# Kernel optimization log

Hardware: AMD Instinct MI355X
Metric: run time of the kernel (lower is better)

The kernel has to match this reference:

```python
import jax, jax.numpy as jnp
import numpy as np

B, LATENT, P, NUM_ATOMS, H, L, E = 16, 128, 16, 64, 64, 4, 32768
N = P * NUM_ATOMS  # 1024

def _lin(k, i, o, s=0.05):
    kw, kb = jax.random.split(k)
    return jax.random.normal(kw, (i, o), jnp.float32) * s, jax.random.normal(kb, (o,), jnp.float32) * s

def setup_inputs() -> dict:
    key = jax.random.key(0)
    ks = jax.random.split(key, 32)
    z = jax.random.normal(ks[0], (B, LATENT), jnp.float32)
    edge_index = jax.random.randint(ks[1], (2, E), 0, N, jnp.int32)
    # build_node_features: (frame/P, atom/num_atoms, 1) per node
    fr = jnp.repeat(jnp.arange(P), NUM_ATOMS) / P
    at = jnp.tile(jnp.arange(NUM_ATOMS), P) / NUM_ATOMS
    node_features = jnp.stack([fr, at, jnp.ones(N)], -1).astype(jnp.float32)
    Wg, bg = _lin(ks[2], LATENT, H)
    Wn, bn = _lin(ks[3], 3, H)
    def stack(fn, base):
        outs = [fn(jax.random.fold_in(key, base + l)) for l in range(L)]
        return tuple(jnp.stack(t) for t in zip(*outs))
    eW1, eb1 = stack(lambda k: _lin(k, 2 * H + 1, H), 100)
    eW2, eb2 = stack(lambda k: _lin(k, H, H), 200)
    cW1, cb1 = stack(lambda k: _lin(k, H, H), 300)
    cW2 = jnp.stack([jax.random.normal(jax.random.fold_in(key, 400 + l), (H, 1), jnp.float32) * 0.05 for l in range(L)])
    nW1, nb1 = stack(lambda k: _lin(k, 2 * H, H), 500)
    nW2, nb2 = stack(lambda k: _lin(k, H, H), 600)
    lng = jnp.ones((L, H), jnp.float32)
    lnb = jnp.zeros((L, H), jnp.float32)
    oW1, ob1 = _lin(ks[4], H, H)
    oW2, ob2 = _lin(ks[5], H, 3)
    return dict(z=z, edge_index=edge_index, node_features=node_features, Wg=Wg, bg=bg, Wn=Wn, bn=bn,
                eW1=eW1, eb1=eb1, eW2=eW2, eb2=eb2, cW1=cW1, cb1=cb1, cW2=cW2,
                nW1=nW1, nb1=nb1, nW2=nW2, nb2=nb2, lng=lng, lnb=lnb,
                oW1=oW1, ob1=ob1, oW2=oW2, ob2=ob2)

def _forward(z, edge_index, node_features, Wg, bg, Wn, bn, eW1, eb1, eW2, eb2,
             cW1, cb1, cW2, nW1, nb1, nW2, nb2, lng, lnb, oW1, ob1, oW2, ob2):
    b = z.shape[0]
    n = node_features.shape[0]
    row, col = edge_index[0], edge_index[1]  # aggregate messages to row
    counts = jnp.clip(jnp.zeros((n,), jnp.float32).at[row].add(1.0), 1.0, None)
    g = z @ Wg + bg                              # [B,H]
    h = (node_features @ Wn + bn)[None] + g[:, None]  # [B,N,H]
    pos = jnp.zeros((b, n, 3), h.dtype)
    for l in range(L):
        hi, hj = h[:, row], h[:, col]            # [B,E,H] gathers
        diff = pos[:, row] - pos[:, col]         # [B,E,3]
        d2 = jnp.sum(diff * diff, -1, keepdims=True)
        m = jax.nn.silu(jnp.concatenate([hi, hj, d2], -1) @ eW1[l] + eb1[l])
        m = jax.nn.silu(m @ eW2[l] + eb2[l])     # [B,E,H]
        w = jax.nn.silu(m @ cW1[l] + cb1[l]) @ cW2[l]  # [B,E,1]
        trans = diff * w
        pos = pos + jnp.zeros_like(pos).at[:, row].add(trans) / counts[None, :, None]
        agg = jnp.zeros_like(h).at[:, row].add(m)      # scatter-sum to nodes
        u = jax.nn.silu(jnp.concatenate([h, agg], -1) @ nW1[l] + nb1[l]) @ nW2[l] + nb2[l]
        h = h + u                                 # node residual
        mu = jnp.mean(h, -1, keepdims=True)
        var = jnp.mean((h - mu) ** 2, -1, keepdims=True)
        h = (h - mu) * jax.lax.rsqrt(var + 1e-5) * lng[l] + lnb[l]
    out = jax.nn.relu(h @ oW1 + ob1) @ oW2 + ob2   # [B,N,3]
    return out.reshape(b, -1)

def reference(z, edge_index, node_features, Wg, bg, Wn, bn, eW1, eb1, eW2, eb2,
              cW1, cb1, cW2, nW1, nb1, nW2, nb2, lng, lnb, oW1, ob1, oW2, ob2):
    return _forward(z, edge_index, node_features, Wg, bg, Wn, bn, eW1, eb1, eW2, eb2,
                    cW1, cb1, cW2, nW1, nb1, nW2, nb2, lng, lnb, oW1, ob1, oW2, ob2)
```

## Files before the change

kernel.cpp:

```cpp
#include <hip/hip_runtime.h>
#include <hip/hip_bf16.h>


namespace {

constexpr int kB = 16, kN = 1024, kH = 64, kE = 32768, kLat = 128;
constexpr int kC = 24;
constexpr int kMaxItems = 2560;

typedef __attribute__((ext_vector_type(8))) short short8;
typedef __attribute__((ext_vector_type(4))) float floatx4;

__device__ __forceinline__ unsigned short f2bf(float f){
  union { float f; unsigned int u; } v; v.f = f;
  unsigned int r = v.u + 0x7fffu + ((v.u >> 16) & 1u);
  return (unsigned short)(r >> 16);
}
__device__ __forceinline__ unsigned int packbf(float a, float b){
  return ((unsigned int)f2bf(b) << 16) | (unsigned int)f2bf(a);
}
__device__ __forceinline__ unsigned int pack2f(float a, float b){
  unsigned int ua = __float_as_uint(a) + 0x8000u;
  unsigned int ub = __float_as_uint(b) + 0x8000u;
  return __builtin_amdgcn_perm(ub, ua, 0x07060302);
}
__device__ __forceinline__ float bflo(unsigned int u){
  union { unsigned int u; float f; } v; v.u = u << 16; return v.f;
}
__device__ __forceinline__ float bfhi(unsigned int u){
  union { unsigned int u; float f; } v; v.u = u & 0xffff0000u; return v.f;
}
__device__ __forceinline__ float silu2(float x){
  float u = __builtin_amdgcn_exp2f(-1.44269504f * x);
  return x * __builtin_amdgcn_rcpf(1.0f + u);
}

__global__ void k_count(const int* ei, int* cntI){
  int e = blockIdx.x*256 + threadIdx.x;
  atomicAdd(&cntI[ei[e]], 1);
}

__global__ void k_scan(const int* cntI, int* off, int* ioff, int* fill,
                       int* items, int* nitems){
  __shared__ int s0[1024];
  __shared__ int s1[1024];
  int t = threadIdx.x;
  int c = cntI[t];
  s0[t] = c; __syncthreads();
  int* src = s0; int* dst = s1;
  for (int o = 1; o < 1024; o <<= 1){
    int v = src[t] + ((t >= o) ? src[t-o] : 0);
    dst[t] = v; __syncthreads();
    int* tmp = src; src = dst; dst = tmp;
  }
  int inc = src[t];
  off[t] = inc - c;
  if (t == 1023) off[1024] = inc;
  fill[t] = 0;
  int ic = (c + (kC-1)) / kC;
  __syncthreads();
  s0[t] = ic; __syncthreads();
  src = s0; dst = s1;
  for (int o = 1; o < 1024; o <<= 1){
    int v = src[t] + ((t >= o) ? src[t-o] : 0);
    dst[t] = v; __syncthreads();
    int* tmp = src; src = dst; dst = tmp;
  }
  int inc2 = src[t];
  int ib = inc2 - ic;
  ioff[t] = ib;
  if (t == 1023){ ioff[1024] = inc2; *nitems = inc2; }
  for (int s = 0; s < ic; s++) items[ib + s] = (t << 12) | s;
}

__global__ void k_bucket(const int* ei, const int* off, int* fill, int* ecol,
                         const float* eW2, unsigned short* wfragE,
                         const float* z, const float* Wg, const float* bg,
                         float* g){
  int e = blockIdx.x*256 + threadIdx.x;
  int r = ei[e];
  int s = atomicAdd(&fill[r], 1);
  ecol[off[r] + s] = ei[kE + e];
  if (blockIdx.x < 4){
    int l = blockIdx.x;
    for (int i = threadIdx.x; i < 4096; i += 256){
      int f = i >> 9, lane = (i >> 3) & 63, j8 = i & 7;
      int jt = f >> 1, ks = f & 1;
      int k = ks*32 + (lane >> 4)*8 + j8;
      int j = jt*16 + (lane & 15);
      wfragE[l*4096 + i] = f2bf(eW2[l*4096 + k*64 + j]);
    }
  } else if (blockIdx.x < 8){
    int b = (blockIdx.x - 4)*4 + (threadIdx.x >> 6);
    int j = threadIdx.x & 63;
    float acc = bg[j];
    for (int k = 0; k < kLat; k++) acc += z[b*kLat + k] * Wg[k*64 + j];
    g[b*64 + j] = acc;
  }
}

__global__ __launch_bounds__(256, 3) void k_pre(const float* nf, const float* Wn,
      const float* bn, const float* g, const float* eW1, const float* eb1,
      float* h, float* A1t, unsigned short* A2bf){
  __shared__ __align__(16) float W0[4096];
  __shared__ __align__(16) float W1[4096];
  __shared__ __align__(16) float HR[16*68];
  __shared__ float b1s[64];
  int tid = threadIdx.x;
  int bb = blockIdx.x >> 6;
  int n0 = (blockIdx.x & 63) * 16;
  {
    const float4* e1a = (const float4*)(eW1);
    const float4* e1b = (const float4*)(eW1 + 4096);
    for (int i = tid; i < 1024; i += 256){ ((float4*)W0)[i] = e1a[i]; ((float4*)W1)[i] = e1b[i]; }
  }
  if (tid < 64) b1s[tid] = eb1[tid];
  int rl = tid >> 4, c = tid & 15, j0 = c*4;
  int n = n0 + rl;
  int row = bb*1024 + n;
  float f0 = nf[n*3], f1 = nf[n*3+1], f2 = nf[n*3+2];
  float4 hv;
  hv.x = f0*Wn[j0+0] + f1*Wn[64+j0+0] + f2*Wn[128+j0+0] + bn[j0+0] + g[bb*64+j0+0];
  hv.y = f0*Wn[j0+1] + f1*Wn[64+j0+1] + f2*Wn[128+j0+1] + bn[j0+1] + g[bb*64+j0+1];
  hv.z = f0*Wn[j0+2] + f1*Wn[64+j0+2] + f2*Wn[128+j0+2] + bn[j0+2] + g[bb*64+j0+2];
  hv.w = f0*Wn[j0+3] + f1*Wn[64+j0+3] + f2*Wn[128+j0+3] + bn[j0+3] + g[bb*64+j0+3];
  *(float4*)(h + row*64 + j0) = hv;
  *(float4*)(HR + rl*68 + j0) = hv;
  __syncthreads();
  float4 a1 = { b1s[j0], b1s[j0+1], b1s[j0+2], b1s[j0+3] };
  float4 a2 = { 0.f, 0.f, 0.f, 0.f };
  #pragma unroll 8
  for (int k = 0; k < 64; k++){
    float hk = HR[rl*68 + k];
    float4 w1 = *(const float4*)(W0 + k*64 + j0);
    float4 w2 = *(const float4*)(W1 + k*64 + j0);
    a1.x += hk*w1.x; a1.y += hk*w1.y; a1.z += hk*w1.z; a1.w += hk*w1.w;
    a2.x += hk*w2.x; a2.y += hk*w2.y; a2.z += hk*w2.z; a2.w += hk*w2.w;
  }
  int tb = (n*16 + bb)*64;
  *(float4*)(A1t + tb + j0) = a1;
  uint2 pk; pk.x = packbf(a2.x, a2.y); pk.y = packbf(a2.z, a2.w);
  *(uint2*)(A2bf + tb + j0) = pk;
}

__global__ __launch_bounds__(256, 3) void k_edge(const float* A1t,
      const unsigned short* A2bf, const unsigned short* wfragE,
      const float* eb2, int l, const int* off, const int* ecol,
      const int* items, const int* nitems, float* P){
  int w = blockIdx.x*4 + (threadIdx.x >> 6);
  if (w >= *nitems) return;
  int lane = threadIdx.x & 63;
  int m = lane & 15, quad = lane >> 4;
  int it = items[w];
  int r = it >> 12, s = it & 4095;
  int e0 = off[r] + s*kC;
  int e1 = min(off[r+1], e0 + kC);

  short8 wf[8];
  #pragma unroll
  for (int f = 0; f < 8; f++)
    wf[f] = *(const short8*)(wfragE + l*4096 + f*512 + lane*8);

  float4 a1[4];
  #pragma unroll
  for (int ks = 0; ks < 2; ks++){
    a1[ks*2+0] = *(const float4*)(A1t + (r<<10) + (m<<6) + ks*32 + quad*8);
    a1[ks*2+1] = *(const float4*)(A1t + (r<<10) + (m<<6) + ks*32 + quad*8 + 4);
  }
  floatx4 dini[4];
  #pragma unroll
  for (int jt = 0; jt < 4; jt++)
    dini[jt] = *(const floatx4*)(eb2 + l*64 + jt*16 + quad*4);
  floatx4 agg[4];
  #pragma unroll
  for (int jt = 0; jt < 4; jt++) agg[jt] = (floatx4){0.f,0.f,0.f,0.f};

  int c0 = ecol[e0];
  uint4 p0 = *(const uint4*)(A2bf + ((c0<<4)+m)*64 + quad*8);
  uint4 p1 = *(const uint4*)(A2bf + ((c0<<4)+m)*64 + 32 + quad*8);

  for (int e = e0; e < e1; e++){
    uint4 c_0 = p0, c_1 = p1;
    if (e + 1 < e1){
      int cn = ecol[e+1];
      p0 = *(const uint4*)(A2bf + ((cn<<4)+m)*64 + quad*8);
      p1 = *(const uint4*)(A2bf + ((cn<<4)+m)*64 + 32 + quad*8);
    }
    short8 bfr[2];
    #pragma unroll
    for (int ks = 0; ks < 2; ks++){
      uint4 a2r = (ks == 0) ? c_0 : c_1;
      float4 x0 = a1[ks*2+0];
      float4 x1 = a1[ks*2+1];
      float v0 = silu2(x0.x + bflo(a2r.x));
      float v1 = silu2(x0.y + bfhi(a2r.x));
      float v2 = silu2(x0.z + bflo(a2r.y));
      float v3 = silu2(x0.w + bfhi(a2r.y));
      float v4 = silu2(x1.x + bflo(a2r.z));
      float v5 = silu2(x1.y + bfhi(a2r.z));
      float v6 = silu2(x1.z + bflo(a2r.w));
      float v7 = silu2(x1.w + bfhi(a2r.w));
      union { uint4 u; short8 s; } bu;
      bu.u.x = pack2f(v0, v1); bu.u.y = pack2f(v2, v3);
      bu.u.z = pack2f(v4, v5); bu.u.w = pack2f(v6, v7);
      bfr[ks] = bu.s;
    }
    #pragma unroll
    for (int jt = 0; jt < 4; jt++){
      floatx4 d = dini[jt];
      d = __builtin_amdgcn_mfma_f32_16x16x32_bf16(wf[jt*2+0], bfr[0], d, 0, 0, 0);
      d = __builtin_amdgcn_mfma_f32_16x16x32_bf16(wf[jt*2+1], bfr[1], d, 0, 0, 0);
      floatx4 a = agg[jt];
      a.x += silu2(d.x); a.y += silu2(d.y);
      a.z += silu2(d.z); a.w += silu2(d.w);
      agg[jt] = a;
    }
  }
  #pragma unroll
  for (int jt = 0; jt < 4; jt++)
    *(floatx4*)(P + w*1024 + m*64 + jt*16 + quad*4) = agg[jt];
}

template <bool LAST>
__global__ __launch_bounds__(256, 3) void k_post(int l, float* h, const float* P,
      const int* ioff, const float* nW1, const float* nb1_, const float* nW2,
      const float* nb2_, const float* lng_, const float* lnb_,
      const float* eW1, const float* eb1_, float* A1t, unsigned short* A2bf,
      const float* oW1, const float* ob1_, const float* oW2, const float* ob2_,
      float* out){
  __shared__ __align__(16) float W0[4096];
  __shared__ __align__(16) float W1[4096];
  __shared__ __align__(16) float HR[16*68];
  __shared__ __align__(16) float AG[16*68];
  __shared__ __align__(16) float TL[16*68];
  __shared__ float b1s[64], b2s[64], lgs[64], lbs[64];
  __shared__ float W2o[192];
  __shared__ float ob2s[4];
  int tid = threadIdx.x;
  int bb = blockIdx.x >> 6;
  int n0 = (blockIdx.x & 63) * 16;
  int rl = tid >> 4, c = tid & 15, j0 = c*4;
  int n = n0 + rl;
  int row = bb*1024 + n;

  {
    const float4* p1 = (const float4*)(nW1 + l*8192);
    const float4* p2 = (const float4*)(nW1 + l*8192 + 4096);
    for (int i = tid; i < 1024; i += 256){ ((float4*)W0)[i] = p1[i]; ((float4*)W1)[i] = p2[i]; }
  }
  if (tid < 64){
    b1s[tid] = nb1_[l*64+tid]; b2s[tid] = nb2_[l*64+tid];
    lgs[tid] = lng_[l*64+tid]; lbs[tid] = lnb_[l*64+tid];
  }
  {
    float4 hv = *(const float4*)(h + row*64 + j0);
    *(float4*)(HR + rl*68 + j0) = hv;
    float4 s = {0.f,0.f,0.f,0.f};
    int i0 = ioff[n], i1 = ioff[n+1];
    for (int i = i0; i < i1; i++){
      float4 v = *(const float4*)(P + i*1024 + bb*64 + j0);
      s.x += v.x; s.y += v.y; s.z += v.z; s.w += v.w;
    }
    *(float4*)(AG + rl*68 + j0) = s;
  }
  __syncthreads();

  float4 t = { b1s[j0], b1s[j0+1], b1s[j0+2], b1s[j0+3] };
  #pragma unroll 8
  for (int k = 0; k < 64; k++){
    float hk = HR[rl*68 + k], ak = AG[rl*68 + k];
    float4 w1 = *(const float4*)(W0 + k*64 + j0);
    float4 w2 = *(const float4*)(W1 + k*64 + j0);
    t.x += hk*w1.x + ak*w2.x; t.y += hk*w1.y + ak*w2.y;
    t.z += hk*w1.z + ak*w2.z; t.w += hk*w1.w + ak*w2.w;
  }
  t.x = silu2(t.x); t.y = silu2(t.y); t.z = silu2(t.z); t.w = silu2(t.w);
  *(float4*)(TL + rl*68 + j0) = t;
  __syncthreads();

  {
    const float4* p3 = (const float4*)(nW2 + l*4096);
    for (int i = tid; i < 1024; i += 256) ((float4*)W0)[i] = p3[i];
  }
  __syncthreads();

  float4 u = { b2s[j0], b2s[j0+1], b2s[j0+2], b2s[j0+3] };
  #pragma unroll 8
  for (int k = 0; k < 64; k++){
    float tk = TL[rl*68 + k];
    float4 w = *(const float4*)(W0 + k*64 + j0);
    u.x += tk*w.x; u.y += tk*w.y; u.z += tk*w.z; u.w += tk*w.w;
  }
  float4 hold = *(const float4*)(HR + rl*68 + j0);
  float4 hv = { hold.x + u.x, hold.y + u.y, hold.z + u.z, hold.w + u.w };
  float s1 = hv.x + hv.y + hv.z + hv.w;
  float s2 = hv.x*hv.x + hv.y*hv.y + hv.z*hv.z + hv.w*hv.w;
  s1 += __shfl_xor(s1, 1, 64); s1 += __shfl_xor(s1, 2, 64);
  s1 += __shfl_xor(s1, 4, 64); s1 += __shfl_xor(s1, 8, 64);
  s2 += __shfl_xor(s2, 1, 64); s2 += __shfl_xor(s2, 2, 64);
  s2 += __shfl_xor(s2, 4, 64); s2 += __shfl_xor(s2, 8, 64);
  float mu  = s1 * (1.0f/64.0f);
  float var = s2 * (1.0f/64.0f) - mu*mu;
  float rs  = rsqrtf(var + 1e-5f);
  float4 hn;
  hn.x = (hv.x-mu)*rs*lgs[j0+0] + lbs[j0+0];
  hn.y = (hv.y-mu)*rs*lgs[j0+1] + lbs[j0+1];
  hn.z = (hv.z-mu)*rs*lgs[j0+2] + lbs[j0+2];
  hn.w = (hv.w-mu)*rs*lgs[j0+3] + lbs[j0+3];
  if (!LAST) *(float4*)(h + row*64 + j0) = hn;
  *(float4*)(HR + rl*68 + j0) = hn;
  __syncthreads();

  if (!LAST){
    {
      const float4* e1a = (const float4*)(eW1 + (l+1)*8256);
      const float4* e1b = (const float4*)(eW1 + (l+1)*8256 + 4096);
      for (int i = tid; i < 1024; i += 256){ ((float4*)W0)[i] = e1a[i]; ((float4*)W1)[i] = e1b[i]; }
    }
    if (tid < 64) b1s[tid] = eb1_[(l+1)*64 + tid];
    __syncthreads();
    float4 a1 = { b1s[j0], b1s[j0+1], b1s[j0+2], b1s[j0+3] };
    float4 a2 = { 0.f, 0.f, 0.f, 0.f };
    #pragma unroll 8
    for (int k = 0; k < 64; k++){
      float hk = HR[rl*68 + k];
      float4 w1 = *(const float4*)(W0 + k*64 + j0);
      float4 w2 = *(const float4*)(W1 + k*64 + j0);
      a1.x += hk*w1.x; a1.y += hk*w1.y; a1.z += hk*w1.z; a1.w += hk*w1.w;
      a2.x += hk*w2.x; a2.y += hk*w2.y; a2.z += hk*w2.z; a2.w += hk*w2.w;
    }
    int tb = (n*16 + bb)*64;
    *(float4*)(A1t + tb + j0) = a1;
    uint2 pk; pk.x = packbf(a2.x, a2.y); pk.y = packbf(a2.z, a2.w);
    *(uint2*)(A2bf + tb + j0) = pk;
  } else {
    {
      const float4* w1p = (const float4*)oW1;
      for (int i = tid; i < 1024; i += 256) ((float4*)W0)[i] = w1p[i];
    }
    if (tid < 192) W2o[tid] = oW2[tid];
    if (tid < 64)  b1s[tid] = ob1_[tid];
    if (tid < 3)   ob2s[tid] = ob2_[tid];
    __syncthreads();
    float4 tr = { b1s[j0], b1s[j0+1], b1s[j0+2], b1s[j0+3] };
    #pragma unroll 8
    for (int k = 0; k < 64; k++){
      float hk = HR[rl*68 + k];
      float4 w = *(const float4*)(W0 + k*64 + j0);
      tr.x += hk*w.x; tr.y += hk*w.y; tr.z += hk*w.z; tr.w += hk*w.w;
    }
    float4 t4 = { fmaxf(tr.x,0.f), fmaxf(tr.y,0.f), fmaxf(tr.z,0.f), fmaxf(tr.w,0.f) };
    *(float4*)(TL + rl*68 + j0) = t4;
    __syncthreads();
    if (c < 3){
      float acc = ob2s[c];
      #pragma unroll 8
      for (int k = 0; k < 64; k++) acc += TL[rl*68 + k] * W2o[k*3 + c];
      out[bb*3072 + n*3 + c] = acc;
    }
  }
}

}

extern "C" void kernel_launch(void* const* d_in, const int* in_sizes, int n_in,
                              void* d_out, int out_size, void* d_ws, size_t ws_size,
                              hipStream_t stream){
  const float* z   = (const float*)d_in[0];
  const int*   ei  = (const int*)d_in[1];
  const float* nf  = (const float*)d_in[2];
  const float* Wg  = (const float*)d_in[3];  const float* bg  = (const float*)d_in[4];
  const float* Wn  = (const float*)d_in[5];  const float* bn  = (const float*)d_in[6];
  const float* eW1 = (const float*)d_in[7];  const float* eb1 = (const float*)d_in[8];
  const float* eW2 = (const float*)d_in[9];  const float* eb2 = (const float*)d_in[10];
  const float* nW1 = (const float*)d_in[14]; const float* nb1 = (const float*)d_in[15];
  const float* nW2 = (const float*)d_in[16]; const float* nb2 = (const float*)d_in[17];
  const float* lng = (const float*)d_in[18]; const float* lnb = (const float*)d_in[19];
  const float* oW1 = (const float*)d_in[20]; const float* ob1 = (const float*)d_in[21];
  const float* oW2 = (const float*)d_in[22]; const float* ob2 = (const float*)d_in[23];

  float* W      = (float*)d_ws;
  float* h      = W;
  float* A1t    = W + 1048576;
  unsigned short* A2bf   = (unsigned short*)(W + 2097152);
  unsigned short* wfragE = (unsigned short*)(W + 2621440);
  float* P      = W + 2629632;
  float* g      = W + 5251072;
  int*   cntI   = (int*)(W + 5252096);
  int*   off    = cntI + 1024;
  int*   ioff   = off + 1025;
  int*   fill   = ioff + 1025;
  int*   items  = fill + 1024;
  int*   nitems = items + 2560;
  int*   ecol   = nitems + 1;

  hipMemsetAsync(cntI, 0, 1024*sizeof(int), stream);
  k_count <<<128, 256, 0, stream>>>(ei, cntI);
  k_scan  <<<1,  1024, 0, stream>>>(cntI, off, ioff, fill, items, nitems);
  k_bucket<<<128, 256, 0, stream>>>(ei, off, fill, ecol, eW2, wfragE, z, Wg, bg, g);
  k_pre   <<<1024, 256, 0, stream>>>(nf, Wn, bn, g, eW1, eb1, h, A1t, A2bf);

  for (int l = 0; l < 4; l++){
    k_edge<<<640, 256, 0, stream>>>(A1t, A2bf, wfragE, eb2, l, off, ecol,
                                    items, nitems, P);
    if (l < 3)
      k_post<false><<<1024, 256, 0, stream>>>(l, h, P, ioff, nW1, nb1, nW2, nb2,
            lng, lnb, eW1, eb1, A1t, A2bf, oW1, ob1, oW2, ob2, (float*)d_out);
    else
      k_post<true> <<<1024, 256, 0, stream>>>(l, h, P, ioff, nW1, nb1, nW2, nb2,
            lng, lnb, eW1, eb1, A1t, A2bf, oW1, ob1, oW2, ob2, (float*)d_out);
  }
}
```

Baseline: 366.9 us.

## Fuse whole forward into one persistent cooperative kernel with grid syncs

Replaces the sequence of count/scan/bucket/pre/edge/post launches with a single cooperative kernel of 768 blocks. Phases are separated by grid-wide syncs and use grid-stride loops over work items. The aim is to remove per-launch overhead and inter-kernel gaps across roughly eleven launches. In exchange, the edge and node phases run on fewer blocks, the scan runs on a single block while the rest wait, and the grid barriers add their own cost. The old multi-kernel path is kept as a fallback if the cooperative launch fails.

```diff
diff --git a/kernel.cpp b/kernel.cpp
--- a/kernel.cpp
+++ b/kernel.cpp
@@ -1,12 +1,15 @@
 #include <hip/hip_runtime.h>
 #include <hip/hip_bf16.h>
+#include <hip/hip_cooperative_groups.h>
+
+namespace cg = cooperative_groups;
 
 
 namespace {
 
 constexpr int kB = 16, kN = 1024, kH = 64, kE = 32768, kLat = 128;
 constexpr int kC = 24;
-constexpr int kMaxItems = 2560;
+constexpr int kGrid = 768;
 
 typedef __attribute__((ext_vector_type(8))) short short8;
 typedef __attribute__((ext_vector_type(4))) float floatx4;
@@ -33,6 +36,326 @@
 __device__ __forceinline__ float silu2(float x){
   float u = __builtin_amdgcn_exp2f(-1.44269504f * x);
   return x * __builtin_amdgcn_rcpf(1.0f + u);
+}
+
+struct Params {
+  const float *z, *nf, *Wg, *bg, *Wn, *bn, *eW1, *eb1, *eW2, *eb2;
+  const float *nW1, *nb1, *nW2, *nb2, *lng, *lnb, *oW1, *ob1, *oW2, *ob2;
+  const int *ei;
+  float *h, *A1t, *P, *g, *out;
+  unsigned short *A2bf, *wfragE;
+  int *cntI, *off, *ioff, *fill, *items, *nitems, *ecol;
+};
+
+__global__ __launch_bounds__(256, 3) void k_all(Params p){
+  __shared__ __align__(16) float W0[4096];
+  __shared__ __align__(16) float W1[4096];
+  __shared__ __align__(16) float HR[16*68];
+  __shared__ __align__(16) float AG[16*68];
+  __shared__ float b1s[64], b2s[64], lgs[64], lbs[64];
+  __shared__ float W2o[192];
+  __shared__ float ob2s[4];
+
+  cg::grid_group gg = cg::this_grid();
+  const int tid = threadIdx.x, blk = blockIdx.x;
+  const int rl = tid >> 4, cc = tid & 15, j0 = cc*4;
+  const int wav = tid >> 6, lane = tid & 63;
+  const int m = lane & 15, quad = lane >> 4;
+
+  for (int e = blk*256 + tid; e < kE; e += kGrid*256)
+    atomicAdd(&p.cntI[p.ei[e]], 1);
+  if (blk < 4){
+    int l = blk;
+    for (int i = tid; i < 4096; i += 256){
+      int f = i >> 9, ln = (i >> 3) & 63, j8 = i & 7;
+      int jt = f >> 1, ks = f & 1;
+      int k = ks*32 + (ln >> 4)*8 + j8;
+      int j = jt*16 + (ln & 15);
+      p.wfragE[l*4096 + i] = f2bf(p.eW2[l*4096 + k*64 + j]);
+    }
+  } else if (blk == 4){
+    int j = tid & 63, b0 = tid >> 6;
+    for (int b = b0; b < 16; b += 4){
+      float acc = p.bg[j];
+      for (int k = 0; k < kLat; k++) acc += p.z[b*kLat + k] * p.Wg[k*64 + j];
+      p.g[b*64 + j] = acc;
+    }
+  }
+  gg.sync();
+
+  if (blk == 0){
+    int* s0 = (int*)W0; int* s1 = s0 + 1024;
+    for (int i = tid; i < 1024; i += 256) s0[i] = p.cntI[i];
+    __syncthreads();
+    int* src = s0; int* dst = s1;
+    for (int o = 1; o < 1024; o <<= 1){
+      for (int i = tid; i < 1024; i += 256)
+        dst[i] = src[i] + ((i >= o) ? src[i-o] : 0);
+      __syncthreads();
+      int* t = src; src = dst; dst = t;
+    }
+    for (int i = tid; i < 1024; i += 256){
+      int c = p.cntI[i];
+      p.off[i] = c ? (src[i] - c) : src[i];
+      p.off[i] = src[i] - c;
+      p.fill[i] = 0;
+    }
+    if (tid == 0) p.off[1024] = src[1023];
+    __syncthreads();
+    for (int i = tid; i < 1024; i += 256) dst[i] = (p.cntI[i] + kC - 1)/kC;
+    __syncthreads();
+    int* src2 = dst; int* dst2 = src;
+    for (int o = 1; o < 1024; o <<= 1){
+      for (int i = tid; i < 1024; i += 256)
+        dst2[i] = src2[i] + ((i >= o) ? src2[i-o] : 0);
+      __syncthreads();
+      int* t = src2; src2 = dst2; dst2 = t;
+    }
+    for (int i = tid; i < 1024; i += 256){
+      int ic = (p.cntI[i] + kC - 1)/kC;
+      int ib = src2[i] - ic;
+      p.ioff[i] = ib;
+      for (int s = 0; s < ic; s++) p.items[ib + s] = (i << 12) | s;
+    }
+    if (tid == 0){ p.ioff[1024] = src2[1023]; p.nitems[0] = src2[1023]; }
+  }
+  gg.sync();
+
+  for (int e = blk*256 + tid; e < kE; e += kGrid*256){
+    int r = p.ei[e];
+    int s = atomicAdd(&p.fill[r], 1);
+    p.ecol[p.off[r] + s] = p.ei[kE + e];
+  }
+  gg.sync();
+
+  {
+    const float4* e1a = (const float4*)(p.eW1);
+    const float4* e1b = (const float4*)(p.eW1 + 4096);
+    for (int i = tid; i < 1024; i += 256){ ((float4*)W0)[i] = e1a[i]; ((float4*)W1)[i] = e1b[i]; }
+    if (tid < 64) b1s[tid] = p.eb1[tid];
+    __syncthreads();
+    for (int grp = blk; grp < 1024; grp += kGrid){
+      int bb = grp >> 6, n0 = (grp & 63)*16;
+      int n = n0 + rl, row = bb*1024 + n;
+      float f0 = p.nf[n*3], f1 = p.nf[n*3+1], f2 = p.nf[n*3+2];
+      float4 hv;
+      hv.x = f0*p.Wn[j0+0] + f1*p.Wn[64+j0+0] + f2*p.Wn[128+j0+0] + p.bn[j0+0] + p.g[bb*64+j0+0];
+      hv.y = f0*p.Wn[j0+1] + f1*p.Wn[64+j0+1] + f2*p.Wn[128+j0+1] + p.bn[j0+1] + p.g[bb*64+j0+1];
+      hv.z = f0*p.Wn[j0+2] + f1*p.Wn[64+j0+2] + f2*p.Wn[128+j0+2] + p.bn[j0+2] + p.g[bb*64+j0+2];
+      hv.w = f0*p.Wn[j0+3] + f1*p.Wn[64+j0+3] + f2*p.Wn[128+j0+3] + p.bn[j0+3] + p.g[bb*64+j0+3];
+      *(float4*)(p.h + row*64 + j0) = hv;
+      *(float4*)(HR + rl*68 + j0) = hv;
+      __syncthreads();
+      float4 a1 = { b1s[j0], b1s[j0+1], b1s[j0+2], b1s[j0+3] };
+      float4 a2 = { 0.f, 0.f, 0.f, 0.f };
+      #pragma unroll 8
+      for (int k = 0; k < 64; k++){
+        float hk = HR[rl*68 + k];
+        float4 w1 = *(const float4*)(W0 + k*64 + j0);
+        float4 w2 = *(const float4*)(W1 + k*64 + j0);
+        a1.x += hk*w1.x; a1.y += hk*w1.y; a1.z += hk*w1.z; a1.w += hk*w1.w;
+        a2.x += hk*w2.x; a2.y += hk*w2.y; a2.z += hk*w2.z; a2.w += hk*w2.w;
+      }
+      int tb = (n*16 + bb)*64;
+      *(float4*)(p.A1t + tb + j0) = a1;
+      uint2 pk2; pk2.x = packbf(a2.x, a2.y); pk2.y = packbf(a2.z, a2.w);
+      *(uint2*)(p.A2bf + tb + j0) = pk2;
+      __syncthreads();
+    }
+  }
+  gg.sync();
+
+  for (int l = 0; l < 4; l++){
+    {
+      short8 wf[8];
+      #pragma unroll
+      for (int f = 0; f < 8; f++)
+        wf[f] = *(const short8*)(p.wfragE + l*4096 + f*512 + lane*8);
+      floatx4 dini[4];
+      #pragma unroll
+      for (int jt = 0; jt < 4; jt++)
+        dini[jt] = *(const floatx4*)(p.eb2 + l*64 + jt*16 + quad*4);
+      int NI = p.nitems[0];
+      for (int w = blk*4 + wav; w < NI; w += kGrid*4){
+        int it = p.items[w];
+        int r = it >> 12, s = it & 4095;
+        int e0 = p.off[r] + s*kC;
+        int e1 = min(p.off[r+1], e0 + kC);
+        float4 a1[4];
+        #pragma unroll
+        for (int ks = 0; ks < 2; ks++){
+          a1[ks*2+0] = *(const float4*)(p.A1t + (r<<10) + (m<<6) + ks*32 + quad*8);
+          a1[ks*2+1] = *(const float4*)(p.A1t + (r<<10) + (m<<6) + ks*32 + quad*8 + 4);
+        }
+        floatx4 agg[4];
+        #pragma unroll
+        for (int jt = 0; jt < 4; jt++) agg[jt] = (floatx4){0.f,0.f,0.f,0.f};
+        int c0 = p.ecol[e0];
+        uint4 p0 = *(const uint4*)(p.A2bf + ((c0<<4)+m)*64 + quad*8);
+        uint4 p1 = *(const uint4*)(p.A2bf + ((c0<<4)+m)*64 + 32 + quad*8);
+        for (int e = e0; e < e1; e++){
+          uint4 c_0 = p0, c_1 = p1;
+          if (e + 1 < e1){
+            int cn = p.ecol[e+1];
+            p0 = *(const uint4*)(p.A2bf + ((cn<<4)+m)*64 + quad*8);
+            p1 = *(const uint4*)(p.A2bf + ((cn<<4)+m)*64 + 32 + quad*8);
+          }
+          short8 bfr[2];
+          #pragma unroll
+          for (int ks = 0; ks < 2; ks++){
+            uint4 a2r = (ks == 0) ? c_0 : c_1;
+            float4 x0 = a1[ks*2+0];
+            float4 x1 = a1[ks*2+1];
+            float v0 = silu2(x0.x + bflo(a2r.x));
+            float v1 = silu2(x0.y + bfhi(a2r.x));
+            float v2 = silu2(x0.z + bflo(a2r.y));
+            float v3 = silu2(x0.w + bfhi(a2r.y));
+            float v4 = silu2(x1.x + bflo(a2r.z));
+            float v5 = silu2(x1.y + bfhi(a2r.z));
+            float v6 = silu2(x1.z + bflo(a2r.w));
+            float v7 = silu2(x1.w + bfhi(a2r.w));
+            union { uint4 u; short8 s; } bu;
+            bu.u.x = pack2f(v0, v1); bu.u.y = pack2f(v2, v3);
+            bu.u.z = pack2f(v4, v5); bu.u.w = pack2f(v6, v7);
+            bfr[ks] = bu.s;
+          }
+          #pragma unroll
+          for (int jt = 0; jt < 4; jt++){
+            floatx4 d = dini[jt];
+            d = __builtin_amdgcn_mfma_f32_16x16x32_bf16(wf[jt*2+0], bfr[0], d, 0, 0, 0);
+            d = __builtin_amdgcn_mfma_f32_16x16x32_bf16(wf[jt*2+1], bfr[1], d, 0, 0, 0);
+            floatx4 a = agg[jt];
+            a.x += silu2(d.x); a.y += silu2(d.y);
+            a.z += silu2(d.z); a.w += silu2(d.w);
+            agg[jt] = a;
+          }
+        }
+        #pragma unroll
+        for (int jt = 0; jt < 4; jt++)
+          *(floatx4*)(p.P + w*1024 + m*64 + jt*16 + quad*4) = agg[jt];
+      }
+    }
+    gg.sync();
+
+    for (int grp = blk; grp < 1024; grp += kGrid){
+      int bb = grp >> 6, n0 = (grp & 63)*16;
+      int n = n0 + rl, row = bb*1024 + n;
+      {
+        const float4* q1 = (const float4*)(p.nW1 + l*8192);
+        const float4* q2 = (const float4*)(p.nW1 + l*8192 + 4096);
+        for (int i = tid; i < 1024; i += 256){ ((float4*)W0)[i] = q1[i]; ((float4*)W1)[i] = q2[i]; }
+        if (tid < 64){
+          b1s[tid] = p.nb1[l*64+tid]; b2s[tid] = p.nb2[l*64+tid];
+          lgs[tid] = p.lng[l*64+tid]; lbs[tid] = p.lnb[l*64+tid];
+        }
+        float4 hv = *(const float4*)(p.h + row*64 + j0);
+        *(float4*)(HR + rl*68 + j0) = hv;
+        float4 s = {0.f,0.f,0.f,0.f};
+        int i0 = p.ioff[n], i1 = p.ioff[n+1];
+        for (int i = i0; i < i1; i++){
+          float4 v = *(const float4*)(p.P + i*1024 + bb*64 + j0);
+          s.x += v.x; s.y += v.y; s.z += v.z; s.w += v.w;
+        }
+        *(float4*)(AG + rl*68 + j0) = s;
+      }
+      __syncthreads();
+      float4 t = { b1s[j0], b1s[j0+1], b1s[j0+2], b1s[j0+3] };
+      #pragma unroll 8
+      for (int k = 0; k < 64; k++){
+        float hk = HR[rl*68 + k], ak = AG[rl*68 + k];
+        float4 w1 = *(const float4*)(W0 + k*64 + j0);
+        float4 w2 = *(const float4*)(W1 + k*64 + j0);
+        t.x += hk*w1.x + ak*w2.x; t.y += hk*w1.y + ak*w2.y;
+        t.z += hk*w1.z + ak*w2.z; t.w += hk*w1.w + ak*w2.w;
+      }
+      t.x = silu2(t.x); t.y = silu2(t.y); t.z = silu2(t.z); t.w = silu2(t.w);
+      __syncthreads();
+      *(float4*)(AG + rl*68 + j0) = t;
+      {
+        const float4* q3 = (const float4*)(p.nW2 + l*4096);
+        for (int i = tid; i < 1024; i += 256) ((float4*)W0)[i] = q3[i];
+      }
+      __syncthreads();
+      float4 u = { b2s[j0], b2s[j0+1], b2s[j0+2], b2s[j0+3] };
+      #pragma unroll 8
+      for (int k = 0; k < 64; k++){
+        float tk = AG[rl*68 + k];
+        float4 w = *(const float4*)(W0 + k*64 + j0);
+        u.x += tk*w.x; u.y += tk*w.y; u.z += tk*w.z; u.w += tk*w.w;
+      }
+      float4 hold = *(const float4*)(HR + rl*68 + j0);
+      float4 hv2 = { hold.x + u.x, hold.y + u.y, hold.z + u.z, hold.w + u.w };
+      float s1 = hv2.x + hv2.y + hv2.z + hv2.w;
+      float s2 = hv2.x*hv2.x + hv2.y*hv2.y + hv2.z*hv2.z + hv2.w*hv2.w;
+      s1 += __shfl_xor(s1, 1, 64); s1 += __shfl_xor(s1, 2, 64);
+      s1 += __shfl_xor(s1, 4, 64); s1 += __shfl_xor(s1, 8, 64);
+      s2 += __shfl_xor(s2, 1, 64); s2 += __shfl_xor(s2, 2, 64);
+      s2 += __shfl_xor(s2, 4, 64); s2 += __shfl_xor(s2, 8, 64);
+      float mu  = s1 * (1.0f/64.0f);
+      float var = s2 * (1.0f/64.0f) - mu*mu;
+      float rs  = rsqrtf(var + 1e-5f);
+      float4 hn;
+      hn.x = (hv2.x-mu)*rs*lgs[j0+0] + lbs[j0+0];
+      hn.y = (hv2.y-mu)*rs*lgs[j0+1] + lbs[j0+1];
+      hn.z = (hv2.z-mu)*rs*lgs[j0+2] + lbs[j0+2];
+      hn.w = (hv2.w-mu)*rs*lgs[j0+3] + lbs[j0+3];
+      if (l < 3) *(float4*)(p.h + row*64 + j0) = hn;
+      __syncthreads();
+      *(float4*)(HR + rl*68 + j0) = hn;
+      if (l < 3){
+        {
+          const float4* e1a = (const float4*)(p.eW1 + (l+1)*8256);
+          const float4* e1b = (const float4*)(p.eW1 + (l+1)*8256 + 4096);
+          for (int i = tid; i < 1024; i += 256){ ((float4*)W0)[i] = e1a[i]; ((float4*)W1)[i] = e1b[i]; }
+        }
+        if (tid < 64) b1s[tid] = p.eb1[(l+1)*64 + tid];
+        __syncthreads();
+        float4 a1 = { b1s[j0], b1s[j0+1], b1s[j0+2], b1s[j0+3] };
+        float4 a2 = { 0.f, 0.f, 0.f, 0.f };
+        #pragma unroll 8
+        for (int k = 0; k < 64; k++){
+          float hk = HR[rl*68 + k];
+          float4 w1 = *(const float4*)(W0 + k*64 + j0);
+          float4 w2 = *(const float4*)(W1 + k*64 + j0);
+          a1.x += hk*w1.x; a1.y += hk*w1.y; a1.z += hk*w1.z; a1.w += hk*w1.w;
+          a2.x += hk*w2.x; a2.y += hk*w2.y; a2.z += hk*w2.z; a2.w += hk*w2.w;
+        }
+        int tb = (n*16 + bb)*64;
+        *(float4*)(p.A1t + tb + j0) = a1;
+        uint2 pk2; pk2.x = packbf(a2.x, a2.y); pk2.y = packbf(a2.z, a2.w);
+        *(uint2*)(p.A2bf + tb + j0) = pk2;
+        __syncthreads();
+      } else {
+        {
+          const float4* w1p = (const float4*)p.oW1;
+          for (int i = tid; i < 1024; i += 256) ((float4*)W0)[i] = w1p[i];
+        }
+        if (tid < 192) W2o[tid] = p.oW2[tid];
+        if (tid < 64)  b1s[tid] = p.ob1[tid];
+        if (tid < 3)   ob2s[tid] = p.ob2[tid];
+        __syncthreads();
+        float4 tr = { b1s[j0], b1s[j0+1], b1s[j0+2], b1s[j0+3] };
+        #pragma unroll 8
+        for (int k = 0; k < 64; k++){
+          float hk = HR[rl*68 + k];
+          float4 w = *(const float4*)(W0 + k*64 + j0);
+          tr.x += hk*w.x; tr.y += hk*w.y; tr.z += hk*w.z; tr.w += hk*w.w;
+        }
+        float4 t4 = { fmaxf(tr.x,0.f), fmaxf(tr.y,0.f), fmaxf(tr.z,0.f), fmaxf(tr.w,0.f) };
+        __syncthreads();
+        *(float4*)(AG + rl*68 + j0) = t4;
+        __syncthreads();
+        if (cc < 3){
+          float acc = ob2s[cc];
+          #pragma unroll 8
+          for (int k = 0; k < 64; k++) acc += AG[rl*68 + k] * W2o[k*3 + cc];
+          p.out[bb*3072 + n*3 + cc] = acc;
+        }
+        __syncthreads();
+      }
+    }
+    if (l < 3) gg.sync();
+  }
 }
 
 __global__ void k_count(const int* ei, int* cntI){
@@ -73,35 +396,30 @@
   for (int s = 0; s < ic; s++) items[ib + s] = (t << 12) | s;
 }
 
-__global__ void k_bucket(const int* ei, const int* off, int* fill, int* ecol,
-                         const float* eW2, unsigned short* wfragE,
-                         const float* z, const float* Wg, const float* bg,
-                         float* g){
+__global__ void k_bucket(Params p){
   int e = blockIdx.x*256 + threadIdx.x;
-  int r = ei[e];
-  int s = atomicAdd(&fill[r], 1);
-  ecol[off[r] + s] = ei[kE + e];
+  int r = p.ei[e];
+  int s = atomicAdd(&p.fill[r], 1);
+  p.ecol[p.off[r] + s] = p.ei[kE + e];
   if (blockIdx.x < 4){
     int l = blockIdx.x;
     for (int i = threadIdx.x; i < 4096; i += 256){
-      int f = i >> 9, lane = (i >> 3) & 63, j8 = i & 7;
+      int f = i >> 9, ln = (i >> 3) & 63, j8 = i & 7;
       int jt = f >> 1, ks = f & 1;
-      int k = ks*32 + (lane >> 4)*8 + j8;
-      int j = jt*16 + (lane & 15);
-      wfragE[l*4096 + i] = f2bf(eW2[l*4096 + k*64 + j]);
+      int k = ks*32 + (ln >> 4)*8 + j8;
+      int j = jt*16 + (ln & 15);
+      p.wfragE[l*4096 + i] = f2bf(p.eW2[l*4096 + k*64 + j]);
     }
   } else if (blockIdx.x < 8){
     int b = (blockIdx.x - 4)*4 + (threadIdx.x >> 6);
     int j = threadIdx.x & 63;
-    float acc = bg[j];
-    for (int k = 0; k < kLat; k++) acc += z[b*kLat + k] * Wg[k*64 + j];
-    g[b*64 + j] = acc;
-  }
-}
-
-__global__ __launch_bounds__(256, 3) void k_pre(const float* nf, const float* Wn,
-      const float* bn, const float* g, const float* eW1, const float* eb1,
-      float* h, float* A1t, unsigned short* A2bf){
+    float acc = p.bg[j];
+    for (int k = 0; k < kLat; k++) acc += p.z[b*kLat + k] * p.Wg[k*64 + j];
+    p.g[b*64 + j] = acc;
+  }
+}
+
+__global__ __launch_bounds__(256, 3) void k_pre(Params p){
   __shared__ __align__(16) float W0[4096];
   __shared__ __align__(16) float W1[4096];
   __shared__ __align__(16) float HR[16*68];
@@ -110,21 +428,21 @@
   int bb = blockIdx.x >> 6;
   int n0 = (blockIdx.x & 63) * 16;
   {
-    const float4* e1a = (const float4*)(eW1);
-    const float4* e1b = (const float4*)(eW1 + 4096);
+    const float4* e1a = (const float4*)(p.eW1);
+    const float4* e1b = (const float4*)(p.eW1 + 4096);
     for (int i = tid; i < 1024; i += 256){ ((float4*)W0)[i] = e1a[i]; ((float4*)W1)[i] = e1b[i]; }
   }
-  if (tid < 64) b1s[tid] = eb1[tid];
+  if (tid < 64) b1s[tid] = p.eb1[tid];
   int rl = tid >> 4, c = tid & 15, j0 = c*4;
   int n = n0 + rl;
   int row = bb*1024 + n;
-  float f0 = nf[n*3], f1 = nf[n*3+1], f2 = nf[n*3+2];
+  float f0 = p.nf[n*3], f1 = p.nf[n*3+1], f2 = p.nf[n*3+2];
   float4 hv;
-  hv.x = f0*Wn[j0+0] + f1*Wn[64+j0+0] + f2*Wn[128+j0+0] + bn[j0+0] + g[bb*64+j0+0];
-  hv.y = f0*Wn[j0+1] + f1*Wn[64+j0+1] + f2*Wn[128+j0+1] + bn[j0+1] + g[bb*64+j0+1];
-  hv.z = f0*Wn[j0+2] + f1*Wn[64+j0+2] + f2*Wn[128+j0+2] + bn[j0+2] + g[bb*64+j0+2];
-  hv.w = f0*Wn[j0+3] + f1*Wn[64+j0+3] + f2*Wn[128+j0+3] + bn[j0+3] + g[bb*64+j0+3];
-  *(float4*)(h + row*64 + j0) = hv;
+  hv.x = f0*p.Wn[j0+0] + f1*p.Wn[64+j0+0] + f2*p.Wn[128+j0+0] + p.bn[j0+0] + p.g[bb*64+j0+0];
+  hv.y = f0*p.Wn[j0+1] + f1*p.Wn[64+j0+1] + f2*p.Wn[128+j0+1] + p.bn[j0+1] + p.g[bb*64+j0+1];
+  hv.z = f0*p.Wn[j0+2] + f1*p.Wn[64+j0+2] + f2*p.Wn[128+j0+2] + p.bn[j0+2] + p.g[bb*64+j0+2];
+  hv.w = f0*p.Wn[j0+3] + f1*p.Wn[64+j0+3] + f2*p.Wn[128+j0+3] + p.bn[j0+3] + p.g[bb*64+j0+3];
+  *(float4*)(p.h + row*64 + j0) = hv;
   *(float4*)(HR + rl*68 + j0) = hv;
   __syncthreads();
   float4 a1 = { b1s[j0], b1s[j0+1], b1s[j0+2], b1s[j0+3] };
@@ -138,53 +456,46 @@
     a2.x += hk*w2.x; a2.y += hk*w2.y; a2.z += hk*w2.z; a2.w += hk*w2.w;
   }
   int tb = (n*16 + bb)*64;
-  *(float4*)(A1t + tb + j0) = a1;
-  uint2 pk; pk.x = packbf(a2.x, a2.y); pk.y = packbf(a2.z, a2.w);
-  *(uint2*)(A2bf + tb + j0) = pk;
-}
-
-__global__ __launch_bounds__(256, 3) void k_edge(const float* A1t,
-      const unsigned short* A2bf, const unsigned short* wfragE,
-      const float* eb2, int l, const int* off, const int* ecol,
-      const int* items, const int* nitems, float* P){
+  *(float4*)(p.A1t + tb + j0) = a1;
+  uint2 pk2; pk2.x = packbf(a2.x, a2.y); pk2.y = packbf(a2.z, a2.w);
+  *(uint2*)(p.A2bf + tb + j0) = pk2;
+}
+
+__global__ __launch_bounds__(256, 3) void k_edge(Params p, int l){
   int w = blockIdx.x*4 + (threadIdx.x >> 6);
-  if (w >= *nitems) return;
+  if (w >= p.nitems[0]) return;
   int lane = threadIdx.x & 63;
   int m = lane & 15, quad = lane >> 4;
-  int it = items[w];
+  int it = p.items[w];
   int r = it >> 12, s = it & 4095;
-  int e0 = off[r] + s*kC;
-  int e1 = min(off[r+1], e0 + kC);
-
+  int e0 = p.off[r] + s*kC;
+  int e1 = min(p.off[r+1], e0 + kC);
   short8 wf[8];
   #pragma unroll
   for (int f = 0; f < 8; f++)
-    wf[f] = *(const short8*)(wfragE + l*4096 + f*512 + lane*8);
-
+    wf[f] = *(const short8*)(p.wfragE + l*4096 + f*512 + lane*8);
   float4 a1[4];
   #pragma unroll
   for (int ks = 0; ks < 2; ks++){
-    a1[ks*2+0] = *(const float4*)(A1t + (r<<10) + (m<<6) + ks*32 + quad*8);
-    a1[ks*2+1] = *(const float4*)(A1t + (r<<10) + (m<<6) + ks*32 + quad*8 + 4);
+    a1[ks*2+0] = *(const float4*)(p.A1t + (r<<10) + (m<<6) + ks*32 + quad*8);
+    a1[ks*2+1] = *(const float4*)(p.A1t + (r<<10) + (m<<6) + ks*32 + quad*8 + 4);
   }
   floatx4 dini[4];
   #pragma unroll
   for (int jt = 0; jt < 4; jt++)
-    dini[jt] = *(const floatx4*)(eb2 + l*64 + jt*16 + quad*4);
+    dini[jt] = *(const floatx4*)(p.eb2 + l*64 + jt*16 + quad*4);
   floatx4 agg[4];
   #pragma unroll
   for (int jt = 0; jt < 4; jt++) agg[jt] = (floatx4){0.f,0.f,0.f,0.f};
-
-  int c0 = ecol[e0];
-  uint4 p0 = *(const uint4*)(A2bf + ((c0<<4)+m)*64 + quad*8);
-  uint4 p1 = *(const uint4*)(A2bf + ((c0<<4)+m)*64 + 32 + quad*8);
-
+  int c0 = p.ecol[e0];
+  uint4 p0 = *(const uint4*)(p.A2bf + ((c0<<4)+m)*64 + quad*8);
+  uint4 p1 = *(const uint4*)(p.A2bf + ((c0<<4)+m)*64 + 32 + quad*8);
   for (int e = e0; e < e1; e++){
     uint4 c_0 = p0, c_1 = p1;
     if (e + 1 < e1){
-      int cn = ecol[e+1];
-      p0 = *(const uint4*)(A2bf + ((cn<<4)+m)*64 + quad*8);
-      p1 = *(const uint4*)(A2bf + ((cn<<4)+m)*64 + 32 + quad*8);
+      int cn = p.ecol[e+1];
+      p0 = *(const uint4*)(p.A2bf + ((cn<<4)+m)*64 + quad*8);
+      p1 = *(const uint4*)(p.A2bf + ((cn<<4)+m)*64 + 32 + quad*8);
     }
     short8 bfr[2];
     #pragma unroll
@@ -218,53 +529,44 @@
   }
   #pragma unroll
   for (int jt = 0; jt < 4; jt++)
-    *(floatx4*)(P + w*1024 + m*64 + jt*16 + quad*4) = agg[jt];
+    *(floatx4*)(p.P + w*1024 + m*64 + jt*16 + quad*4) = agg[jt];
 }
 
 template <bool LAST>
-__global__ __launch_bounds__(256, 3) void k_post(int l, float* h, const float* P,
-      const int* ioff, const float* nW1, const float* nb1_, const float* nW2,
-      const float* nb2_, const float* lng_, const float* lnb_,
-      const float* eW1, const float* eb1_, float* A1t, unsigned short* A2bf,
-      const float* oW1, const float* ob1_, const float* oW2, const float* ob2_,
-      float* out){
+__global__ __launch_bounds__(256, 3) void k_post(Params p, int l){
   __shared__ __align__(16) float W0[4096];
   __shared__ __align__(16) float W1[4096];
   __shared__ __align__(16) float HR[16*68];
   __shared__ __align__(16) float AG[16*68];
-  __shared__ __align__(16) float TL[16*68];
   __shared__ float b1s[64], b2s[64], lgs[64], lbs[64];
   __shared__ float W2o[192];
   __shared__ float ob2s[4];
   int tid = threadIdx.x;
   int bb = blockIdx.x >> 6;
   int n0 = (blockIdx.x & 63) * 16;
-  int rl = tid >> 4, c = tid & 15, j0 = c*4;
-  int n = n0 + rl;
-  int row = bb*1024 + n;
-
+  int rl = tid >> 4, cc = tid & 15, j0 = cc*4;
+  int n = n0 + rl, row = bb*1024 + n;
   {
-    const float4* p1 = (const float4*)(nW1 + l*8192);
-    const float4* p2 = (const float4*)(nW1 + l*8192 + 4096);
-    for (int i = tid; i < 1024; i += 256){ ((float4*)W0)[i] = p1[i]; ((float4*)W1)[i] = p2[i]; }
+    const float4* q1 = (const float4*)(p.nW1 + l*8192);
+    const float4* q2 = (const float4*)(p.nW1 + l*8192 + 4096);
+    for (int i = tid; i < 1024; i += 256){ ((float4*)W0)[i] = q1[i]; ((float4*)W1)[i] = q2[i]; }
   }
   if (tid < 64){
-    b1s[tid] = nb1_[l*64+tid]; b2s[tid] = nb2_[l*64+tid];
-    lgs[tid] = lng_[l*64+tid]; lbs[tid] = lnb_[l*64+tid];
+    b1s[tid] = p.nb1[l*64+tid]; b2s[tid] = p.nb2[l*64+tid];
+    lgs[tid] = p.lng[l*64+tid]; lbs[tid] = p.lnb[l*64+tid];
   }
   {
-    float4 hv = *(const float4*)(h + row*64 + j0);
+    float4 hv = *(const float4*)(p.h + row*64 + j0);
     *(float4*)(HR + rl*68 + j0) = hv;
     float4 s = {0.f,0.f,0.f,0.f};
-    int i0 = ioff[n], i1 = ioff[n+1];
+    int i0 = p.ioff[n], i1 = p.ioff[n+1];
     for (int i = i0; i < i1; i++){
-      float4 v = *(const float4*)(P + i*1024 + bb*64 + j0);
+      float4 v = *(const float4*)(p.P + i*1024 + bb*64 + j0);
       s.x += v.x; s.y += v.y; s.z += v.z; s.w += v.w;
     }
     *(float4*)(AG + rl*68 + j0) = s;
   }
   __syncthreads();
-
   float4 t = { b1s[j0], b1s[j0+1], b1s[j0+2], b1s[j0+3] };
   #pragma unroll 8
   for (int k = 0; k < 64; k++){
@@ -275,26 +577,24 @@
     t.z += hk*w1.z + ak*w2.z; t.w += hk*w1.w + ak*w2.w;
   }
   t.x = silu2(t.x); t.y = silu2(t.y); t.z = silu2(t.z); t.w = silu2(t.w);
-  *(float4*)(TL + rl*68 + j0) = t;
   __syncthreads();
-
+  *(float4*)(AG + rl*68 + j0) = t;
   {
-    const float4* p3 = (const float4*)(nW2 + l*4096);
-    for (int i = tid; i < 1024; i += 256) ((float4*)W0)[i] = p3[i];
+    const float4* q3 = (const float4*)(p.nW2 + l*4096);
+    for (int i = tid; i < 1024; i += 256) ((float4*)W0)[i] = q3[i];
   }
   __syncthreads();
-
   float4 u = { b2s[j0], b2s[j0+1], b2s[j0+2], b2s[j0+3] };
   #pragma unroll 8
   for (int k = 0; k < 64; k++){
-    float tk = TL[rl*68 + k];
+    float tk = AG[rl*68 + k];
     float4 w = *(const float4*)(W0 + k*64 + j0);
     u.x += tk*w.x; u.y += tk*w.y; u.z += tk*w.z; u.w += tk*w.w;
   }
   float4 hold = *(const float4*)(HR + rl*68 + j0);
-  float4 hv = { hold.x + u.x, hold.y + u.y, hold.z + u.z, hold.w + u.w };
-  float s1 = hv.x + hv.y + hv.z + hv.w;
-  float s2 = hv.x*hv.x + hv.y*hv.y + hv.z*hv.z + hv.w*hv.w;
+  float4 hv2 = { hold.x + u.x, hold.y + u.y, hold.z + u.z, hold.w + u.w };
+  float s1 = hv2.x + hv2.y + hv2.z + hv2.w;
+  float s2 = hv2.x*hv2.x + hv2.y*hv2.y + hv2.z*hv2.z + hv2.w*hv2.w;
   s1 += __shfl_xor(s1, 1, 64); s1 += __shfl_xor(s1, 2, 64);
   s1 += __shfl_xor(s1, 4, 64); s1 += __shfl_xor(s1, 8, 64);
   s2 += __shfl_xor(s2, 1, 64); s2 += __shfl_xor(s2, 2, 64);
@@ -303,21 +603,20 @@
   float var = s2 * (1.0f/64.0f) - mu*mu;
   float rs  = rsqrtf(var + 1e-5f);
   float4 hn;
-  hn.x = (hv.x-mu)*rs*lgs[j0+0] + lbs[j0+0];
-  hn.y = (hv.y-mu)*rs*lgs[j0+1] + lbs[j0+1];
-  hn.z = (hv.z-mu)*rs*lgs[j0+2] + lbs[j0+2];
-  hn.w = (hv.w-mu)*rs*lgs[j0+3] + lbs[j0+3];
-  if (!LAST) *(float4*)(h + row*64 + j0) = hn;
+  hn.x = (hv2.x-mu)*rs*lgs[j0+0] + lbs[j0+0];
+  hn.y = (hv2.y-mu)*rs*lgs[j0+1] + lbs[j0+1];
+  hn.z = (hv2.z-mu)*rs*lgs[j0+2] + lbs[j0+2];
+  hn.w = (hv2.w-mu)*rs*lgs[j0+3] + lbs[j0+3];
+  if (!LAST) *(float4*)(p.h + row*64 + j0) = hn;
+  __syncthreads();
   *(float4*)(HR + rl*68 + j0) = hn;
-  __syncthreads();
-
   if (!LAST){
     {
-      const float4* e1a = (const float4*)(eW1 + (l+1)*8256);
-      const float4* e1b = (const float4*)(eW1 + (l+1)*8256 + 4096);
+      const float4* e1a = (const float4*)(p.eW1 + (l+1)*8256);
+      const float4* e1b = (const float4*)(p.eW1 + (l+1)*8256 + 4096);
       for (int i = tid; i < 1024; i += 256){ ((float4*)W0)[i] = e1a[i]; ((float4*)W1)[i] = e1b[i]; }
     }
-    if (tid < 64) b1s[tid] = eb1_[(l+1)*64 + tid];
+    if (tid < 64) b1s[tid] = p.eb1[(l+1)*64 + tid];
     __syncthreads();
     float4 a1 = { b1s[j0], b1s[j0+1], b1s[j0+2], b1s[j0+3] };
     float4 a2 = { 0.f, 0.f, 0.f, 0.f };
@@ -330,17 +629,17 @@
       a2.x += hk*w2.x; a2.y += hk*w2.y; a2.z += hk*w2.z; a2.w += hk*w2.w;
     }
     int tb = (n*16 + bb)*64;
-    *(float4*)(A1t + tb + j0) = a1;
-    uint2 pk; pk.x = packbf(a2.x, a2.y); pk.y = packbf(a2.z, a2.w);
-    *(uint2*)(A2bf + tb + j0) = pk;
+    *(float4*)(p.A1t + tb + j0) = a1;
+    uint2 pk2; pk2.x = packbf(a2.x, a2.y); pk2.y = packbf(a2.z, a2.w);
+    *(uint2*)(p.A2bf + tb + j0) = pk2;
   } else {
     {
-      const float4* w1p = (const float4*)oW1;
+      const float4* w1p = (const float4*)p.oW1;
       for (int i = tid; i < 1024; i += 256) ((float4*)W0)[i] = w1p[i];
     }
-    if (tid < 192) W2o[tid] = oW2[tid];
-    if (tid < 64)  b1s[tid] = ob1_[tid];
-    if (tid < 3)   ob2s[tid] = ob2_[tid];
+    if (tid < 192) W2o[tid] = p.oW2[tid];
+    if (tid < 64)  b1s[tid] = p.ob1[tid];
+    if (tid < 3)   ob2s[tid] = p.ob2[tid];
     __syncthreads();
     float4 tr = { b1s[j0], b1s[j0+1], b1s[j0+2], b1s[j0+3] };
     #pragma unroll 8
@@ -350,13 +649,14 @@
       tr.x += hk*w.x; tr.y += hk*w.y; tr.z += hk*w.z; tr.w += hk*w.w;
     }
     float4 t4 = { fmaxf(tr.x,0.f), fmaxf(tr.y,0.f), fmaxf(tr.z,0.f), fmaxf(tr.w,0.f) };
-    *(float4*)(TL + rl*68 + j0) = t4;
     __syncthreads();
-    if (c < 3){
-      float acc = ob2s[c];
+    *(float4*)(AG + rl*68 + j0) = t4;
+    __syncthreads();
+    if (cc < 3){
+      float acc = ob2s[cc];
       #pragma unroll 8
-      for (int k = 0; k < 64; k++) acc += TL[rl*68 + k] * W2o[k*3 + c];
-      out[bb*3072 + n*3 + c] = acc;
+      for (int k = 0; k < 64; k++) acc += AG[rl*68 + k] * W2o[k*3 + cc];
+      p.out[bb*3072 + n*3 + cc] = acc;
     }
   }
 }
@@ -366,48 +666,50 @@
 extern "C" void kernel_launch(void* const* d_in, const int* in_sizes, int n_in,
                               void* d_out, int out_size, void* d_ws, size_t ws_size,
                               hipStream_t stream){
-  const float* z   = (const float*)d_in[0];
-  const int*   ei  = (const int*)d_in[1];
-  const float* nf  = (const float*)d_in[2];
-  const float* Wg  = (const float*)d_in[3];  const float* bg  = (const float*)d_in[4];
-  const float* Wn  = (const float*)d_in[5];  const float* bn  = (const float*)d_in[6];
-  const float* eW1 = (const float*)d_in[7];  const float* eb1 = (const float*)d_in[8];
-  const float* eW2 = (const float*)d_in[9];  const float* eb2 = (const float*)d_in[10];
-  const float* nW1 = (const float*)d_in[14]; const float* nb1 = (const float*)d_in[15];
-  const float* nW2 = (const float*)d_in[16]; const float* nb2 = (const float*)d_in[17];
-  const float* lng = (const float*)d_in[18]; const float* lnb = (const float*)d_in[19];
-  const float* oW1 = (const float*)d_in[20]; const float* ob1 = (const float*)d_in[21];
-  const float* oW2 = (const float*)d_in[22]; const float* ob2 = (const float*)d_in[23];
-
-  float* W      = (float*)d_ws;
-  float* h      = W;
-  float* A1t    = W + 1048576;
-  unsigned short* A2bf   = (unsigned short*)(W + 2097152);
-  unsigned short* wfragE = (unsigned short*)(W + 2621440);
-  float* P      = W + 2629632;
-  float* g      = W + 5251072;
-  int*   cntI   = (int*)(W + 5252096);
-  int*   off    = cntI + 1024;
-  int*   ioff   = off + 1025;
-  int*   fill   = ioff + 1025;
-  int*   items  = fill + 1024;
-  int*   nitems = items + 2560;
-  int*   ecol   = nitems + 1;
-
-  hipMemsetAsync(cntI, 0, 1024*sizeof(int), stream);
-  k_count <<<128, 256, 0, stream>>>(ei, cntI);
-  k_scan  <<<1,  1024, 0, stream>>>(cntI, off, ioff, fill, items, nitems);
-  k_bucket<<<128, 256, 0, stream>>>(ei, off, fill, ecol, eW2, wfragE, z, Wg, bg, g);
-  k_pre   <<<1024, 256, 0, stream>>>(nf, Wn, bn, g, eW1, eb1, h, A1t, A2bf);
-
-  for (int l = 0; l < 4; l++){
-    k_edge<<<640, 256, 0, stream>>>(A1t, A2bf, wfragE, eb2, l, off, ecol,
-                                    items, nitems, P);
-    if (l < 3)
-      k_post<false><<<1024, 256, 0, stream>>>(l, h, P, ioff, nW1, nb1, nW2, nb2,
-            lng, lnb, eW1, eb1, A1t, A2bf, oW1, ob1, oW2, ob2, (float*)d_out);
-    else
-      k_post<true> <<<1024, 256, 0, stream>>>(l, h, P, ioff, nW1, nb1, nW2, nb2,
-            lng, lnb, eW1, eb1, A1t, A2bf, oW1, ob1, oW2, ob2, (float*)d_out);
-  }
-}
+  float* W = (float*)d_ws;
+  Params p;
+  p.z   = (const float*)d_in[0];
+  p.ei  = (const int*)d_in[1];
+  p.nf  = (const float*)d_in[2];
+  p.Wg  = (const float*)d_in[3];  p.bg  = (const float*)d_in[4];
+  p.Wn  = (const float*)d_in[5];  p.bn  = (const float*)d_in[6];
+  p.eW1 = (const float*)d_in[7];  p.eb1 = (const float*)d_in[8];
+  p.eW2 = (const float*)d_in[9];  p.eb2 = (const float*)d_in[10];
+  p.nW1 = (const float*)d_in[14]; p.nb1 = (const float*)d_in[15];
+  p.nW2 = (const float*)d_in[16]; p.nb2 = (const float*)d_in[17];
+  p.lng = (const float*)d_in[18]; p.lnb = (const float*)d_in[19];
+  p.oW1 = (const float*)d_in[20]; p.ob1 = (const float*)d_in[21];
+  p.oW2 = (const float*)d_in[22]; p.ob2 = (const float*)d_in[23];
+  p.out = (float*)d_out;
+
+  p.h      = W;
+  p.A1t    = W + 1048576;
+  p.A2bf   = (unsigned short*)(W + 2097152);
+  p.wfragE = (unsigned short*)(W + 2621440);
+  p.P      = W + 2629632;
+  p.g      = W + 5251072;
+  p.cntI   = (int*)(W + 5252096);
+  p.off    = p.cntI + 1024;
+  p.ioff   = p.off + 1025;
+  p.fill   = p.ioff + 1025;
+  p.items  = p.fill + 1024;
+  p.nitems = p.items + 2560;
+  p.ecol   = p.nitems + 1;
+
+  hipMemsetAsync(p.cntI, 0, 1024*sizeof(int), stream);
+
+  void* kargs[] = { (void*)&p };
+  hipError_t err = hipLaunchCooperativeKernel(k_all, dim3(kGrid), dim3(256),
+                                              kargs, 0, stream);
+  if (err != hipSuccess){
+    k_count <<<128, 256, 0, stream>>>(p.ei, p.cntI);
+    k_scan  <<<1,  1024, 0, stream>>>(p.cntI, p.off, p.ioff, p.fill, p.items, p.nitems);
+    k_bucket<<<128, 256, 0, stream>>>(p);
+    k_pre   <<<1024, 256, 0, stream>>>(p);
+    for (int l = 0; l < 4; l++){
+      k_edge<<<640, 256, 0, stream>>>(p, l);
+      if (l < 3) k_post<false><<<1024, 256, 0, stream>>>(p, l);
+      else       k_post<true> <<<1024, 256, 0, stream>>>(p, l);
+    }
+  }
+}
```

New measurement: 1.304 ms. 256% more time.
